# Performance work log

Measured on AMD Instinct MI355X. Metric: run time of the kernel, lower is better.

The kernel has to match this reference:

```python
import jax, jax.numpy as jnp
import numpy as np

N_LAYERS = 11
DILATIONS = tuple(2 ** i for i in range(N_LAYERS))   # 1..1024
MEM_SIZES = DILATIONS                                 # kernel=2 -> 1 past tap -> mem = dilation
HOP = 128
C_SCALE = 1.0
FFT = 256       # channel width
NUM_CLS = 256   # mu-law classes
COND = 80       # mel bands
FRAMES = 16


def setup_inputs() -> dict:
    key = jax.random.key(0)
    ks = jax.random.split(key, 10)
    s = 0.05  # keep logits well-scaled for softmax sampling
    return {
        "y": jax.random.normal(ks[0], (COND, FRAMES), jnp.float32),
        "samples": jax.random.uniform(ks[1], (FRAMES * HOP,), jnp.float32),
        "emb_raw": jax.random.normal(ks[2], (NUM_CLS, FFT), jnp.float32) * 0.5,
        "condition_W": jax.random.normal(ks[3], (N_LAYERS * FFT, COND), jnp.float32) * s,
        "WV_past": jax.random.normal(ks[4], (N_LAYERS, FFT, FFT, 1), jnp.float32) * s,
        "WV_present": jax.random.normal(ks[5], (N_LAYERS, FFT, FFT), jnp.float32) * s,
        "W_o_w": jax.random.normal(ks[6], (N_LAYERS, FFT, FFT), jnp.float32) * s,
        "W_o_b": jax.random.normal(ks[7], (N_LAYERS, FFT), jnp.float32) * s,
        "end_w": jax.random.normal(ks[8], (NUM_CLS, FFT), jnp.float32) * s,
        "end_b": jax.random.normal(ks[9], (NUM_CLS,), jnp.float32) * s,
    }


def reference(y, samples, emb_raw, condition_W, WV_past, WV_present, W_o_w, W_o_b, end_w, end_b):
    emb = jnp.tanh(emb_raw)                      # fftnet.emb[0].weight.tanh()
    T = y.shape[1] * HOP
    # F.interpolate nearest with scale_factor=hop_length == frame repeat
    yu = jnp.repeat(y, HOP, axis=1)              # [COND, T]
    # precompute all conditioning projections (condition_W @ y[:, i], chunked per layer)
    conds = (condition_W @ yu).reshape(N_LAYERS, FFT, T).transpose(2, 0, 1)  # [T, L, FFT]

    bufs0 = tuple(jnp.zeros((FFT, m), jnp.float32) for m in MEM_SIZES)
    x0 = emb[NUM_CLS // 2 - 1]
    n_taps = WV_past.shape[3]

    def step(carry, inp):
        x, bufs = carry
        cond_t, u, t = inp
        new_bufs = []
        for j in range(N_LAYERS):
            mem = bufs[j]
            m = MEM_SIZES[j]
            idx = t % m                                   # ring-buffer write/oldest-read ptr
            h = cond_t[j]
            ii = idx
            for k in range(n_taps):                       # read past taps (before write)
                h = h + WV_past[j, :, :, k] @ mem[:, ii]
                ii = (ii + DILATIONS[j]) % m
            h = h + WV_present[j] @ x
            new_bufs.append(mem.at[:, idx].set(x))        # write current x into ring buffer
            h = jax.nn.relu(h)
            z = W_o_w[j] @ h + W_o_b[j]
            x = jax.nn.relu(z + x)                        # residual + relu
        logits = (end_w @ x + end_b) * C_SCALE
        cum = jnp.cumsum(jax.nn.softmax(logits))
        new_idx = jnp.argmax(cum > u)                     # nonzero(cum > u)[0]
        return (emb[new_idx], tuple(new_bufs)), new_idx

    ts = jnp.arange(T)
    _, outputs = jax.lax.scan(step, (x0, bufs0), (conds, samples, ts))
    return outputs  # [T] int sampled mu-law classes
```

## Files before the change

kernel.cpp:

```cpp
#include <hip/hip_runtime.h>
#include <math.h>


#define T_STEPS 2048
#define NBLK    53

typedef unsigned long long u64;
typedef float v64f __attribute__((ext_vector_type(64)));

#define OFF_EMBT   0
#define OFF_WPET   65536
#define OFF_WVPET  131072
#define OFF_RINGS  196608
#define OFF_TAPQ   1244672
#define OFF_ZQ4    1408512
#define OFF_XQ     1431040
#define OFF_IDXQ   1436672
#define WS_FLOATS  1436736

#define FBAR(r)  (32*(r))

__device__ __forceinline__ float ldc(const float* p) {
  int v = __hip_atomic_load((const int*)p, __ATOMIC_RELAXED, __HIP_MEMORY_SCOPE_AGENT);
  return __int_as_float(v);
}
__device__ __forceinline__ void stc(float* p, float x) {
  __hip_atomic_store((int*)p, __float_as_int(x), __ATOMIC_RELAXED, __HIP_MEMORY_SCOPE_AGENT);
}
__device__ __forceinline__ u64 ldq(const u64* p) {
  return __hip_atomic_load(p, __ATOMIC_RELAXED, __HIP_MEMORY_SCOPE_AGENT);
}
__device__ __forceinline__ void stq(u64* p, float v, int tag) {
  u64 x = (u64)(unsigned)__float_as_int(v) | ((u64)(unsigned)tag << 32);
  __hip_atomic_store(p, x, __ATOMIC_RELAXED, __HIP_MEMORY_SCOPE_AGENT);
}
__device__ __forceinline__ int ptag(u64 q) { return (int)(q >> 32); }
__device__ __forceinline__ float pval(u64 q) { return __int_as_float((int)(unsigned)q); }

__device__ __forceinline__ float spin_pair(const u64* p, int want) {
  int bud = 1 << 20; u64 q;
  do { q = ldq(p); } while (ptag(q) < want && --bud > 0);
  return pval(q);
}
__device__ __forceinline__ int spin_idx(const u64* p, int want) {
  int bud = 1 << 20; u64 q;
  do { q = ldq(p); } while (ptag(q) < want && --bud > 0);
  return __float_as_int(pval(q)) & 255;
}
__device__ __forceinline__ void spin3(const u64* p1, const u64* p2, const u64* p3,
                                      int want, float& v1, float& v2, float& v3) {
  int bud = 1 << 20; u64 q1, q2, q3; bool ok;
  do {
    q1 = ldq(p1); q2 = ldq(p2); q3 = ldq(p3);
    ok = (ptag(q1) >= want) & (ptag(q2) >= want) & (ptag(q3) >= want);
  } while (!ok && --bud > 0);
  v1 = pval(q1); v2 = pval(q2); v3 = pval(q3);
}
__device__ __forceinline__ void spin5(const u64* p0, const u64* p1, const u64* p2,
                                      const u64* p3, const u64* p4, int want,
                                      float& v0, float& v1, float& v2, float& v3, float& v4) {
  int bud = 1 << 20; u64 q0, q1, q2, q3, q4; bool ok;
  do {
    q0 = ldq(p0); q1 = ldq(p1); q2 = ldq(p2); q3 = ldq(p3); q4 = ldq(p4);
    ok = (ptag(q0) >= want) & (ptag(q1) >= want) & (ptag(q2) >= want)
       & (ptag(q3) >= want) & (ptag(q4) >= want);
  } while (!ok && --bud > 0);
  v0 = pval(q0); v1 = pval(q1); v2 = pval(q2); v3 = pval(q3); v4 = pval(q4);
}
__device__ __forceinline__ void spin_tag2(const u64* p1, const u64* p2, int w1, int w2) {
  int bud = 1 << 20; u64 q1, q2; bool ok;
  do {
    q1 = ldq(p1); q2 = ldq(p2);
    ok = (ptag(q1) >= w1) & (ptag(q2) >= w2);
  } while (!ok && --bud > 0);
}
__device__ __forceinline__ void wait1(int* f, int want) {
  int it = 0;
  while (__hip_atomic_load(f, __ATOMIC_RELAXED, __HIP_MEMORY_SCOPE_AGENT) < want) {
    if (++it > (1 << 22)) break;
  }
  (void)__hip_atomic_load(f, __ATOMIC_ACQUIRE, __HIP_MEMORY_SCOPE_AGENT);
}
__device__ __forceinline__ void post(int* f, int v) {
  __hip_atomic_store(f, v, __ATOMIC_RELEASE, __HIP_MEMORY_SCOPE_AGENT);
}

__global__ __launch_bounds__(512, 1)
void fftnet_kernel(const float* __restrict__ y, const float* __restrict__ samples,
                   const float* __restrict__ emb_raw, const float* __restrict__ condW,
                   const float* __restrict__ WV_past, const float* __restrict__ WV_present,
                   const float* __restrict__ W_o_w, const float* __restrict__ W_o_b,
                   const float* __restrict__ end_w, const float* __restrict__ end_b,
                   int* __restrict__ out, float* __restrict__ ws)
{
  const int tid = threadIdx.x;
  const int bid = blockIdx.x;
  int* iflags = (int*)(ws + WS_FLOATS);
  u64* zq4  = (u64*)(ws + OFF_ZQ4);
  u64* xq   = (u64*)(ws + OFF_XQ);
  u64* tq   = (u64*)(ws + OFF_TAPQ);
  u64* idxq = (u64*)(ws + OFF_IDXQ);

  __shared__ float s_x[256];
  __shared__ float s_h[256];
  __shared__ float s_p[1024];
  __shared__ float s_cond[2048];
  __shared__ float s_tap[64];
  __shared__ float s_m[320];
  __shared__ unsigned long long s_mask[8];

  for (int i = bid * 512 + tid; i < 65536; i += NBLK * 512)
    stc(ws + OFF_EMBT + i, tanhf(emb_raw[i]));
  __syncthreads();
  if (tid == 0) post(iflags + FBAR(bid), 1);
  if (tid < NBLK) wait1(iflags + FBAR(tid), 1);
  __syncthreads();

  for (int n = bid; n < 512; n += NBLK) {
    const float* wmat = (n < 256) ? WV_present : WV_past;
    int cls = n & 255;
    int c = tid & 255, s2 = tid >> 8;
    float acc = 0.f;
    for (int k = 128 * s2; k < 128 * s2 + 128; ++k)
      acc += wmat[c * 256 + k] * ws[OFF_EMBT + cls * 256 + k];
    s_p[s2 * 256 + c] = acc;
    __syncthreads();
    if (tid < 256)
      stc(ws + ((n < 256) ? OFF_WPET : OFF_WVPET) + cls * 256 + tid, s_p[tid] + s_p[256 + tid]);
    __syncthreads();
  }
  __syncthreads();
  if (tid == 0) post(iflags + FBAR(bid), 2);
  if (tid < NBLK) wait1(iflags + FBAR(tid), 2);
  __syncthreads();
  __builtin_amdgcn_fence(__ATOMIC_ACQUIRE, "agent");
  __syncthreads();

  if (bid == 0) {
    const int c = tid & 255, s2 = tid >> 8;
    v64f we0, we1;
#pragma unroll
    for (int i = 0; i < 64; ++i) we0[i] = end_w[c * 256 + 128 * s2 + i];
#pragma unroll
    for (int i = 0; i < 64; ++i) we1[i] = end_w[c * 256 + 128 * s2 + 64 + i];
    const float eb = end_b[c];
    const float b10 = W_o_b[10 * 256 + c];
    const u64* pz0 = zq4 + (10 * 4 + 0) * 256;
    const u64* pz1 = zq4 + (10 * 4 + 1) * 256;
    const u64* pz2 = zq4 + (10 * 4 + 2) * 256;
    const u64* pz3 = zq4 + (10 * 4 + 3) * 256;
    const u64* pxq = xq + 10 * 256;
    const int lane = tid & 63, w = tid >> 6;
    if (tid == 0) stq(idxq, __int_as_float(127), 1);

    for (int t = 0; t < T_STEPS; ++t) {
      float u = samples[t];
      if (tid < 256) {
        float a, b, cc, d, r3;
        spin5(pz0 + tid, pz1 + tid, pz2 + tid, pz3 + tid, pxq + tid, t + 1, a, b, cc, d, r3);
        float s01 = a + b, s23 = cc + d;
        s_x[tid] = fmaxf(s01 + s23 + b10 + r3, 0.f);
      }
      __syncthreads();
      float acc = 0.f;
#pragma unroll
      for (int i = 0; i < 64; ++i) acc += we0[i] * s_x[128 * s2 + i];
#pragma unroll
      for (int i = 0; i < 64; ++i) acc += we1[i] * s_x[128 * s2 + 64 + i];
      s_p[s2 * 256 + c] = acc;
      __syncthreads();
      float logit = 0.f;
      if (tid < 256) logit = s_p[tid] + s_p[256 + tid] + eb;
      float vmax = (tid < 256) ? logit : -3.4e38f;
#pragma unroll
      for (int d2 = 32; d2 > 0; d2 >>= 1) vmax = fmaxf(vmax, __shfl_xor(vmax, d2, 64));
      if (lane == 0) s_m[280 + w] = vmax;
      __syncthreads();
      float mx = fmaxf(fmaxf(s_m[280], s_m[281]), fmaxf(s_m[282], s_m[283]));
      float e = (tid < 256) ? expf(logit - mx) : 0.f;
      float vs = e;
#pragma unroll
      for (int d2 = 32; d2 > 0; d2 >>= 1) vs += __shfl_xor(vs, d2, 64);
      if (lane == 0) s_m[288 + w] = vs;
      __syncthreads();
      float ssum = s_m[288] + s_m[289] + s_m[290] + s_m[291];
      float p = (tid < 256) ? (e / ssum) : 0.f;
      float v = p;
#pragma unroll
      for (int d2 = 1; d2 < 64; d2 <<= 1) {
        float o = __shfl_up(v, (unsigned)d2, 64);
        if (lane >= d2) v += o;
      }
      if (tid < 256 && lane == 63) s_m[256 + w] = v;
      __syncthreads();
      float offs = 0.f;
      if (tid < 256) for (int k = 0; k < w; ++k) offs += s_m[256 + k];
      float cum = v + offs;
      unsigned long long msk = __ballot(tid < 256 && (cum > u));
      if (lane == 0) s_mask[w] = msk;
      __syncthreads();
      if (tid == 0) {
        int idx = 0;
        for (int k = 0; k < 4; ++k) {
          unsigned long long m2 = s_mask[k];
          if (m2) { idx = k * 64 + (int)__builtin_ctzll(m2); break; }
        }
        stq(idxq, __int_as_float(idx), t + 2);
        out[t] = idx;
      }
      __syncthreads();
    }

  } else if (bid <= 2) {
    const int side = bid - 1;
    const int row = tid & 255, chunk = tid >> 8;
    v64f wv;
#pragma unroll
    for (int i = 0; i < 64; ++i)
      wv[i] = W_o_w[row * 256 + side * 128 + chunk * 64 + i];
    for (int e = tid; e < 2048; e += 512) {
      int f = e >> 7, rr = e & 127;
      float a = 0.f;
      for (int q = 0; q < 80; ++q) a += condW[(side * 128 + rr) * 80 + q] * y[q * 16 + f];
      s_cond[f * 128 + rr] = a;
    }
    __syncthreads();
    u64* zout = zq4 + (0 * 4 + side) * 256;
    int pidx = 127;

    for (int t = 0; t < T_STEPS; ++t) {
      int idx = pidx;
      if (tid < 128) {
        float tapv = (t > 0) ? ws[OFF_WVPET + pidx * 256 + side * 128 + tid] : 0.f;
        idx = spin_idx(idxq, t + 1);
        float hv = s_cond[(t >> 7) * 128 + tid]
                 + ws[OFF_WPET + idx * 256 + side * 128 + tid] + tapv;
        s_h[tid] = fmaxf(hv, 0.f);
        if (tid == 0) s_m[300] = __int_as_float(idx);
      }
      __syncthreads();
      float acc = 0.f;
#pragma unroll
      for (int i = 0; i < 64; ++i) acc += wv[i] * s_h[64 * chunk + i];
      s_p[chunk * 256 + row] = acc;
      __syncthreads();
      if (tid < 256) stq(zout + tid, s_p[tid] + s_p[256 + tid], t + 1);
      pidx = (tid < 128) ? idx : __float_as_int(s_m[300]);
      __syncthreads();
    }

  } else if (bid <= 42) {
    const int jj = 1 + ((bid - 3) >> 2);
    const int k  = (bid - 3) & 3;
    v64f wv;
    if (tid < 256) {
      int r = tid & 63, s = tid >> 6;
#pragma unroll
      for (int i = 0; i < 64; ++i)
        wv[i] = WV_present[jj * 65536 + (64 * k + r) * 256 + 64 * s + i];
    } else {
      int row = tid - 256;
#pragma unroll
      for (int i = 0; i < 64; ++i)
        wv[i] = W_o_w[jj * 65536 + row * 256 + 64 * k + i];
    }
    const float bprev = W_o_b[(jj - 1) * 256 + (tid & 255)];
    for (int e = tid; e < 1024; e += 512) {
      int f = e >> 6, rr = e & 63;
      float a = 0.f;
      for (int q = 0; q < 80; ++q)
        a += condW[(jj * 256 + 64 * k + rr) * 80 + q] * y[q * 16 + f];
      s_cond[f * 64 + rr] = a;
    }
    __syncthreads();
    const int dj = 1 << jj, maskj = 2 * dj - 1;
    float* ringj = ws + OFF_RINGS + 512 * (dj - 1);
    const u64* pz0 = zq4 + ((jj - 1) * 4 + 0) * 256;
    const u64* pz1 = zq4 + ((jj - 1) * 4 + 1) * 256;
    const u64* pz2 = zq4 + ((jj - 1) * 4 + 2) * 256;
    const u64* pz3 = zq4 + ((jj - 1) * 4 + 3) * 256;
    const u64* pxp = xq + (jj - 1) * 256;
    u64* zout = zq4 + (jj * 4 + k) * 256;
    u64* xout = xq + jj * 256;
    const u64* ptap = tq + (jj - 1) * 32 * 256;

    for (int t = 0; t < T_STEPS; ++t) {
      const int want = t + 1;
      if (tid < 256) {
        float xv;
        if (jj == 1) {
          float a, b, iv;
          spin3(pz0 + tid, pz1 + tid, idxq, want, a, b, iv);
          int idx = __float_as_int(iv) & 255;
          xv = fmaxf((a + b) + bprev + ws[OFF_EMBT + idx * 256 + tid], 0.f);
        } else {
          float a, b, cc, d, xp;
          spin5(pz0 + tid, pz1 + tid, pz2 + tid, pz3 + tid, pxp + tid, want, a, b, cc, d, xp);
          float s01 = a + b, s23 = cc + d;
          xv = fmaxf(s01 + s23 + bprev + xp, 0.f);
        }
        s_x[tid] = xv;
        if (k == 0) stq(xout + tid, xv, want);
      } else if (tid >= 384 && tid < 448) {
        int l = tid - 384;
        s_tap[l] = spin_pair(ptap + (t & 31) * 256 + 64 * k + l, want);
      }
      __syncthreads();
      if (tid < 256) {
        int r = tid & 63, s = tid >> 6;
        float acc = 0.f;
#pragma unroll
        for (int i = 0; i < 64; ++i) acc += wv[i] * s_x[64 * s + i];
        s_p[s * 64 + r] = acc;
      } else if (k == 0) {
        int row = tid - 256;
        stc(ringj + (t & maskj) * 256 + row, s_x[row]);
      }
      __syncthreads();
      if (tid < 64) {
        float hv = s_p[tid] + s_p[64 + tid] + s_p[128 + tid] + s_p[192 + tid]
                 + s_cond[(t >> 7) * 64 + tid] + s_tap[tid];
        s_h[tid] = fmaxf(hv, 0.f);
      }
      __syncthreads();
      if (tid >= 256) {
        int row = tid - 256;
        float acc = 0.f;
#pragma unroll
        for (int i = 0; i < 64; ++i) acc += wv[i] * s_h[i];
        if (k == 0)
          __builtin_amdgcn_fence(__ATOMIC_RELEASE, "agent");
        stq(zout + row, acc, want);
      }
      __syncthreads();
    }

  } else {
    const int j = bid - 42;
    const int dj = 1 << j, maskj = 2 * dj - 1;
    v64f wq0, wq1;
    { int r = tid & 255, s2 = tid >> 8;
#pragma unroll
      for (int i = 0; i < 64; ++i) wq0[i] = WV_past[j * 65536 + r * 256 + 128 * s2 + i];
#pragma unroll
      for (int i = 0; i < 64; ++i) wq1[i] = WV_past[j * 65536 + r * 256 + 128 * s2 + 64 + i]; }
    float* ringj = ws + OFF_RINGS + 512 * (dj - 1);
    u64* tapj = tq + (j - 1) * 32 * 256;
    const u64* z0 = zq4 + (j * 4 + 0) * 256;

    for (int t = 0; t < T_STEPS; ++t) {
      int g0 = t - 31;
      if (t >= dj && t - dj + 1 > g0) g0 = t - dj + 1;
      int gk = t - 31;
      if (tid < 256 && (g0 >= 1 || gk >= 1)) {
        const u64* zk = zq4 + (j * 4 + (tid >> 6)) * 256;
        spin_tag2(z0 + tid, zk + tid, g0, gk);
      }
      float tapv = 0.f;
      if (t >= dj) {
        if (tid < 256) s_x[tid] = ldc(ringj + ((t - dj) & maskj) * 256 + tid);
        __syncthreads();
        int r = tid & 255, s2 = tid >> 8;
        float acc = 0.f;
#pragma unroll
        for (int i = 0; i < 64; ++i) acc += wq0[i] * s_x[128 * s2 + i];
#pragma unroll
        for (int i = 0; i < 64; ++i) acc += wq1[i] * s_x[128 * s2 + 64 + i];
        s_p[s2 * 256 + r] = acc;
        __syncthreads();
        if (tid < 256) tapv = s_p[tid] + s_p[256 + tid];
      }
      if (tid < 256) stq(tapj + (t & 31) * 256 + tid, tapv, t + 1);
      __syncthreads();
    }
  }
}

extern "C" void kernel_launch(void* const* d_in, const int* in_sizes, int n_in,
                              void* d_out, int out_size, void* d_ws, size_t ws_size,
                              hipStream_t stream) {
  const float* y       = (const float*)d_in[0];
  const float* samples = (const float*)d_in[1];
  const float* emb_raw = (const float*)d_in[2];
  const float* condW   = (const float*)d_in[3];
  const float* WV_past = (const float*)d_in[4];
  const float* WV_pres = (const float*)d_in[5];
  const float* W_o_w   = (const float*)d_in[6];
  const float* W_o_b   = (const float*)d_in[7];
  const float* end_w   = (const float*)d_in[8];
  const float* end_b   = (const float*)d_in[9];
  (void)in_sizes; (void)n_in; (void)out_size; (void)ws_size;
  hipLaunchKernelGGL(fftnet_kernel, dim3(NBLK), dim3(512), 0, stream,
                     y, samples, emb_raw, condW, WV_past, WV_pres,
                     W_o_w, W_o_b, end_w, end_b, (int*)d_out, (float*)d_ws);
}
```

Before: 50.48 ms.

## Fold layer-0 output projection into the layer-1 blocks, removing two blocks

Drops the two dedicated layer-0 blocks that computed the W_o projection and published partial z values through global queues. Each of the four layer-1 blocks now redundantly computes the full layer-0 hidden state, its 256x256 projection and the residual locally, then continues with its layer-1 work. This removes one cross-block global-memory handoff with its spin-wait from the per-step critical path, and cuts the block count. In exchange each layer-1 block carries more registers (two extra 64-float weight vectors) and a larger shared conditioning buffer, and does redundant layer-0 work.

```diff
diff --git a/kernel.cpp b/kernel.cpp
--- a/kernel.cpp
+++ b/kernel.cpp
@@ -3,7 +3,7 @@
 
 
 #define T_STEPS 2048
-#define NBLK    53
+#define NBLK    51
 
 typedef unsigned long long u64;
 typedef float v64f __attribute__((ext_vector_type(64)));
@@ -46,15 +46,6 @@
   int bud = 1 << 20; u64 q;
   do { q = ldq(p); } while (ptag(q) < want && --bud > 0);
   return __float_as_int(pval(q)) & 255;
-}
-__device__ __forceinline__ void spin3(const u64* p1, const u64* p2, const u64* p3,
-                                      int want, float& v1, float& v2, float& v3) {
-  int bud = 1 << 20; u64 q1, q2, q3; bool ok;
-  do {
-    q1 = ldq(p1); q2 = ldq(p2); q3 = ldq(p3);
-    ok = (ptag(q1) >= want) & (ptag(q2) >= want) & (ptag(q3) >= want);
-  } while (!ok && --bud > 0);
-  v1 = pval(q1); v2 = pval(q2); v3 = pval(q3);
 }
 __device__ __forceinline__ void spin5(const u64* p0, const u64* p1, const u64* p2,
                                       const u64* p3, const u64* p4, int want,
@@ -104,7 +95,7 @@
   __shared__ float s_x[256];
   __shared__ float s_h[256];
   __shared__ float s_p[1024];
-  __shared__ float s_cond[2048];
+  __shared__ float s_cond[5120];
   __shared__ float s_tap[64];
   __shared__ float s_m[320];
   __shared__ unsigned long long s_mask[8];
@@ -211,47 +202,9 @@
       __syncthreads();
     }
 
-  } else if (bid <= 2) {
-    const int side = bid - 1;
-    const int row = tid & 255, chunk = tid >> 8;
-    v64f wv;
-#pragma unroll
-    for (int i = 0; i < 64; ++i)
-      wv[i] = W_o_w[row * 256 + side * 128 + chunk * 64 + i];
-    for (int e = tid; e < 2048; e += 512) {
-      int f = e >> 7, rr = e & 127;
-      float a = 0.f;
-      for (int q = 0; q < 80; ++q) a += condW[(side * 128 + rr) * 80 + q] * y[q * 16 + f];
-      s_cond[f * 128 + rr] = a;
-    }
-    __syncthreads();
-    u64* zout = zq4 + (0 * 4 + side) * 256;
-    int pidx = 127;
-
-    for (int t = 0; t < T_STEPS; ++t) {
-      int idx = pidx;
-      if (tid < 128) {
-        float tapv = (t > 0) ? ws[OFF_WVPET + pidx * 256 + side * 128 + tid] : 0.f;
-        idx = spin_idx(idxq, t + 1);
-        float hv = s_cond[(t >> 7) * 128 + tid]
-                 + ws[OFF_WPET + idx * 256 + side * 128 + tid] + tapv;
-        s_h[tid] = fmaxf(hv, 0.f);
-        if (tid == 0) s_m[300] = __int_as_float(idx);
-      }
-      __syncthreads();
-      float acc = 0.f;
-#pragma unroll
-      for (int i = 0; i < 64; ++i) acc += wv[i] * s_h[64 * chunk + i];
-      s_p[chunk * 256 + row] = acc;
-      __syncthreads();
-      if (tid < 256) stq(zout + tid, s_p[tid] + s_p[256 + tid], t + 1);
-      pidx = (tid < 128) ? idx : __float_as_int(s_m[300]);
-      __syncthreads();
-    }
-
-  } else if (bid <= 42) {
-    const int jj = 1 + ((bid - 3) >> 2);
-    const int k  = (bid - 3) & 3;
+  } else if (bid <= 40) {
+    const int jj = 1 + ((bid - 1) >> 2);
+    const int k  = (bid - 1) & 3;
     v64f wv;
     if (tid < 256) {
       int r = tid & 63, s = tid >> 6;
@@ -264,79 +217,151 @@
       for (int i = 0; i < 64; ++i)
         wv[i] = W_o_w[jj * 65536 + row * 256 + 64 * k + i];
     }
-    const float bprev = W_o_b[(jj - 1) * 256 + (tid & 255)];
     for (int e = tid; e < 1024; e += 512) {
       int f = e >> 6, rr = e & 63;
       float a = 0.f;
       for (int q = 0; q < 80; ++q)
         a += condW[(jj * 256 + 64 * k + rr) * 80 + q] * y[q * 16 + f];
-      s_cond[f * 64 + rr] = a;
+      s_cond[4096 + f * 64 + rr] = a;
     }
-    __syncthreads();
     const int dj = 1 << jj, maskj = 2 * dj - 1;
     float* ringj = ws + OFF_RINGS + 512 * (dj - 1);
-    const u64* pz0 = zq4 + ((jj - 1) * 4 + 0) * 256;
-    const u64* pz1 = zq4 + ((jj - 1) * 4 + 1) * 256;
-    const u64* pz2 = zq4 + ((jj - 1) * 4 + 2) * 256;
-    const u64* pz3 = zq4 + ((jj - 1) * 4 + 3) * 256;
-    const u64* pxp = xq + (jj - 1) * 256;
     u64* zout = zq4 + (jj * 4 + k) * 256;
     u64* xout = xq + jj * 256;
     const u64* ptap = tq + (jj - 1) * 32 * 256;
 
-    for (int t = 0; t < T_STEPS; ++t) {
-      const int want = t + 1;
-      if (tid < 256) {
-        float xv;
-        if (jj == 1) {
-          float a, b, iv;
-          spin3(pz0 + tid, pz1 + tid, idxq, want, a, b, iv);
-          int idx = __float_as_int(iv) & 255;
-          xv = fmaxf((a + b) + bprev + ws[OFF_EMBT + idx * 256 + tid], 0.f);
-        } else {
+    if (jj == 1) {
+      v64f w00, w01;
+      { int c = tid & 255, s2 = tid >> 8;
+#pragma unroll
+        for (int i = 0; i < 64; ++i) w00[i] = W_o_w[c * 256 + 128 * s2 + i];
+#pragma unroll
+        for (int i = 0; i < 64; ++i) w01[i] = W_o_w[c * 256 + 128 * s2 + 64 + i]; }
+      const float b0 = W_o_b[tid & 255];
+      for (int e = tid; e < 4096; e += 512) {
+        int f = e >> 8, r = e & 255;
+        float a = 0.f;
+        for (int q = 0; q < 80; ++q) a += condW[r * 80 + q] * y[q * 16 + f];
+        s_cond[f * 256 + r] = a;
+      }
+      __syncthreads();
+      int pidx = 127;
+
+      for (int t = 0; t < T_STEPS; ++t) {
+        const int want = t + 1;
+        if (tid < 256) {
+          float wvp = (t > 0) ? ws[OFF_WVPET + pidx * 256 + tid] : 0.f;
+          int idx = spin_idx(idxq, want);
+          float x0 = ws[OFF_EMBT + idx * 256 + tid];
+          float h0 = s_cond[(t >> 7) * 256 + tid] + ws[OFF_WPET + idx * 256 + tid] + wvp;
+          s_h[tid] = fmaxf(h0, 0.f);
+          s_x[tid] = x0;
+          pidx = idx;
+        } else if (tid >= 384 && tid < 448) {
+          int l = tid - 384;
+          s_tap[l] = spin_pair(ptap + (t & 31) * 256 + 64 * k + l, want);
+        }
+        __syncthreads();
+        {
+          int c = tid & 255, s2 = tid >> 8;
+          float a0 = 0.f, a1 = 0.f;
+#pragma unroll
+          for (int i = 0; i < 64; ++i) a0 += w00[i] * s_h[128 * s2 + i];
+#pragma unroll
+          for (int i = 0; i < 64; ++i) a1 += w01[i] * s_h[128 * s2 + 64 + i];
+          s_p[s2 * 256 + c] = a0 + a1;
+        }
+        __syncthreads();
+        if (tid < 256) {
+          float x1 = fmaxf((s_p[tid] + s_p[256 + tid]) + b0 + s_x[tid], 0.f);
+          s_x[tid] = x1;
+          if (k == 0) stq(xout + tid, x1, want);
+        }
+        __syncthreads();
+        if (tid < 256) {
+          int r = tid & 63, s = tid >> 6;
+          float acc = 0.f;
+#pragma unroll
+          for (int i = 0; i < 64; ++i) acc += wv[i] * s_x[64 * s + i];
+          s_p[s * 64 + r] = acc;
+        } else if (k == 0) {
+          int row = tid - 256;
+          stc(ringj + (t & maskj) * 256 + row, s_x[row]);
+        }
+        __syncthreads();
+        if (tid < 64) {
+          float hv = s_p[tid] + s_p[64 + tid] + s_p[128 + tid] + s_p[192 + tid]
+                   + s_cond[4096 + (t >> 7) * 64 + tid] + s_tap[tid];
+          s_h[tid] = fmaxf(hv, 0.f);
+        }
+        __syncthreads();
+        if (tid >= 256) {
+          int row = tid - 256;
+          float acc = 0.f;
+#pragma unroll
+          for (int i = 0; i < 64; ++i) acc += wv[i] * s_h[i];
+          if (k == 0)
+            __builtin_amdgcn_fence(__ATOMIC_RELEASE, "agent");
+          stq(zout + row, acc, want);
+        }
+        __syncthreads();
+      }
+
+    } else {
+      const float bprev = W_o_b[(jj - 1) * 256 + (tid & 255)];
+      __syncthreads();
+      const u64* pz0 = zq4 + ((jj - 1) * 4 + 0) * 256;
+      const u64* pz1 = zq4 + ((jj - 1) * 4 + 1) * 256;
+      const u64* pz2 = zq4 + ((jj - 1) * 4 + 2) * 256;
+      const u64* pz3 = zq4 + ((jj - 1) * 4 + 3) * 256;
+      const u64* pxp = xq + (jj - 1) * 256;
+
+      for (int t = 0; t < T_STEPS; ++t) {
+        const int want = t + 1;
+        if (tid < 256) {
           float a, b, cc, d, xp;
           spin5(pz0 + tid, pz1 + tid, pz2 + tid, pz3 + tid, pxp + tid, want, a, b, cc, d, xp);
           float s01 = a + b, s23 = cc + d;
-          xv = fmaxf(s01 + s23 + bprev + xp, 0.f);
-        }
-        s_x[tid] = xv;
-        if (k == 0) stq(xout + tid, xv, want);
-      } else if (tid >= 384 && tid < 448) {
-        int l = tid - 384;
-        s_tap[l] = spin_pair(ptap + (t & 31) * 256 + 64 * k + l, want);
-      }
-      __syncthreads();
-      if (tid < 256) {
-        int r = tid & 63, s = tid >> 6;
-        float acc = 0.f;
-#pragma unroll
-        for (int i = 0; i < 64; ++i) acc += wv[i] * s_x[64 * s + i];
-        s_p[s * 64 + r] = acc;
-      } else if (k == 0) {
-        int row = tid - 256;
-        stc(ringj + (t & maskj) * 256 + row, s_x[row]);
-      }
-      __syncthreads();
-      if (tid < 64) {
-        float hv = s_p[tid] + s_p[64 + tid] + s_p[128 + tid] + s_p[192 + tid]
-                 + s_cond[(t >> 7) * 64 + tid] + s_tap[tid];
-        s_h[tid] = fmaxf(hv, 0.f);
-      }
-      __syncthreads();
-      if (tid >= 256) {
-        int row = tid - 256;
-        float acc = 0.f;
-#pragma unroll
-        for (int i = 0; i < 64; ++i) acc += wv[i] * s_h[i];
-        if (k == 0)
-          __builtin_amdgcn_fence(__ATOMIC_RELEASE, "agent");
-        stq(zout + row, acc, want);
-      }
-      __syncthreads();
+          float xv = fmaxf(s01 + s23 + bprev + xp, 0.f);
+          s_x[tid] = xv;
+          if (k == 0) stq(xout + tid, xv, want);
+        } else if (tid >= 384 && tid < 448) {
+          int l = tid - 384;
+          s_tap[l] = spin_pair(ptap + (t & 31) * 256 + 64 * k + l, want);
+        }
+        __syncthreads();
+        if (tid < 256) {
+          int r = tid & 63, s = tid >> 6;
+          float acc = 0.f;
+#pragma unroll
+          for (int i = 0; i < 64; ++i) acc += wv[i] * s_x[64 * s + i];
+          s_p[s * 64 + r] = acc;
+        } else if (k == 0) {
+          int row = tid - 256;
+          stc(ringj + (t & maskj) * 256 + row, s_x[row]);
+        }
+        __syncthreads();
+        if (tid < 64) {
+          float hv = s_p[tid] + s_p[64 + tid] + s_p[128 + tid] + s_p[192 + tid]
+                   + s_cond[4096 + (t >> 7) * 64 + tid] + s_tap[tid];
+          s_h[tid] = fmaxf(hv, 0.f);
+        }
+        __syncthreads();
+        if (tid >= 256) {
+          int row = tid - 256;
+          float acc = 0.f;
+#pragma unroll
+          for (int i = 0; i < 64; ++i) acc += wv[i] * s_h[i];
+          if (k == 0)
+            __builtin_amdgcn_fence(__ATOMIC_RELEASE, "agent");
+          stq(zout + row, acc, want);
+        }
+        __syncthreads();
+      }
     }
 
   } else {
-    const int j = bid - 42;
+    const int j = bid - 40;
     const int dj = 1 << j, maskj = 2 * dj - 1;
     v64f wq0, wq1;
     { int r = tid & 255, s2 = tid >> 8;
```

Result: slower. 52.67 ms (+4.3%).
